# Performance work log

Hardware: AMD Instinct MI355X
Metric: run time of the kernel (lower is better)

## Reference

```python
import jax, jax.numpy as jnp
import numpy as np

N_NODES = 100000
N_EDGES = 3200000
F_IN = 256
H1 = 128   # growth_rate * bn_size
H2 = 32    # growth_rate
BN_EPS = 1e-5


def _gin_bn_relu(x, edge_index, Wa, ba, Wb, bb, gamma, beta):
    # GINConv (eps=0): h_i = MLP(x_i + sum_{j in N(i)} x_j)
    src, dst = edge_index[0], edge_index[1]
    agg = jax.ops.segment_sum(x[src], dst, num_segments=x.shape[0])  # [N, F]
    h = x + agg
    # nn1: Linear -> ReLU -> Linear
    h = jnp.maximum(h @ Wa + ba, 0.0)
    h = h @ Wb + bb
    # BatchNorm1d (training-mode batch stats over nodes)
    mean = h.mean(axis=0)
    var = h.var(axis=0)  # biased, matches torch BN normalization
    h = (h - mean) * jax.lax.rsqrt(var + BN_EPS) * gamma + beta
    return jnp.maximum(h, 0.0)


def setup_inputs() -> dict:
    key = jax.random.key(0)
    ks = jax.random.split(key, 12)
    x = jax.random.normal(ks[0], (N_NODES, F_IN), dtype=jnp.float32)
    edge_index = jax.random.randint(ks[1], (2, N_EDGES), 0, N_NODES, dtype=jnp.int64)

    def lin(k, fin, fout):
        s = 1.0 / np.sqrt(fin)
        return jax.random.uniform(k, (fin, fout), jnp.float32, -s, s)

    return {
        "x": x,
        "edge_index": edge_index,
        "W1a": lin(ks[2], F_IN, H1), "b1a": jnp.zeros((H1,), jnp.float32),
        "W1b": lin(ks[3], H1, H1),   "b1b": jnp.zeros((H1,), jnp.float32),
        "g1": jnp.ones((H1,), jnp.float32), "be1": jnp.zeros((H1,), jnp.float32),
        "W2a": lin(ks[4], H1, H2),   "b2a": jnp.zeros((H2,), jnp.float32),
        "W2b": lin(ks[5], H2, H2),   "b2b": jnp.zeros((H2,), jnp.float32),
        "g2": jnp.ones((H2,), jnp.float32), "be2": jnp.zeros((H2,), jnp.float32),
    }


def reference(x, edge_index, W1a, b1a, W1b, b1b, g1, be1,
              W2a, b2a, W2b, b2b, g2, be2):
    # data.x is a single tensor -> [x]; torch.cat([x], 1) == x (concat is a no-op)
    h = _gin_bn_relu(x, edge_index, W1a, b1a, W1b, b1b, g1, be1)   # [N, 128]
    h = _gin_bn_relu(h, edge_index, W2a, b2a, W2b, b2b, g2, be2)   # [N, 32]
    return h
```

## Files before the change

kernel.cpp:

```cpp
#include <hip/hip_runtime.h>

#define F_IN 256
#define H1 128
#define H2 32
#define BN_EPS 1e-5f
#define BSHIFT 8
#define BCAP 16384
#define CHUNK 4096
#define NSHARD 8

typedef short bf16x8 __attribute__((ext_vector_type(8)));
typedef float f32x4 __attribute__((ext_vector_type(4)));

__device__ __forceinline__ ushort f2bf(float f) {
    uint u = __float_as_uint(f);
    return (ushort)((u + 0x7FFFu + ((u >> 16) & 1u)) >> 16);
}
__device__ __forceinline__ float bf2f(ushort h) {
    return __uint_as_float((uint)h << 16);
}
__device__ __forceinline__ uint pack2(float a, float b) {
    return (uint)f2bf(a) | ((uint)f2bf(b) << 16);
}
__device__ __forceinline__ void unpack2(uint u, float& a, float& b) {
    a = __uint_as_float(u << 16);
    b = __uint_as_float(u & 0xFFFF0000u);
}
__device__ __forceinline__ int clampN(int v, int N) {
    return v < 0 ? 0 : (v >= N ? N - 1 : v);
}

__global__ __launch_bounds__(256) void super0_k(
    const float* __restrict__ W1a, const float* __restrict__ W1b,
    const float* __restrict__ W2a, const float* __restrict__ W2b,
    ushort* __restrict__ w1aT, ushort* __restrict__ w1bT,
    ushort* __restrict__ w2aT, ushort* __restrict__ w2bT,
    int* __restrict__ bucket_cursor, float* __restrict__ sums1,
    float* __restrict__ sums2) {
    const int tid = threadIdx.x;
    if (blockIdx.x == 212) {
        for (int i = tid; i < 512; i += 256) bucket_cursor[i] = 0;
        for (int i = tid; i < NSHARD * 2 * H1; i += 256) sums1[i] = 0.f;
        for (int i = tid; i < NSHARD * 2 * H2; i += 256) sums2[i] = 0.f;
        return;
    }
    int idx = blockIdx.x * 256 + tid;
    if (idx < 32768) {
        int k = idx >> 7, c = idx & 127;
        w1aT[c * 256 + k] = f2bf(W1a[idx]);
    } else if (idx < 49152) {
        int t = idx - 32768;
        int k = t >> 7, c = t & 127;
        w1bT[c * 128 + k] = f2bf(W1b[t]);
    } else if (idx < 53248) {
        int t = idx - 49152;
        int k = t >> 5, c = t & 31;
        w2aT[c * 128 + k] = f2bf(W2a[t]);
    } else if (idx < 54272) {
        int t = idx - 53248;
        int k = t >> 5, c = t & 31;
        w2bT[c * 32 + k] = f2bf(W2b[t]);
    }
}

__global__ __launch_bounds__(256) void binA_k(const int* __restrict__ eb,
                                              int E, int N, int NBUCK,
                                              int* __restrict__ bucket_cursor,
                                              uint* __restrict__ rec) {
    __shared__ int lcnt[512];
    __shared__ int lbase[512];
    __shared__ uint lrec[CHUNK];
    __shared__ ushort lbk[CHUNK];
    __shared__ ushort lrk[CHUNK];
    __shared__ int nzf;
    const int tid = threadIdx.x;
    const int cbase = blockIdx.x * CHUNK;
    const int cnum = min(CHUNK, E - cbase);
    if (cnum <= 0) return;
    if (tid == 0) nzf = 0;
    __syncthreads();
    {
        int i = tid * (CHUNK / 256);
        if (i < cnum && eb[2 * (cbase + i) + 1] != 0) atomicAdd(&nzf, 1);
    }
    for (int i = tid; i < NBUCK; i += 256) lcnt[i] = 0;
    __syncthreads();
    const int is64 = (nzf == 0);
    for (int i = tid; i < cnum; i += 256) {
        int e = cbase + i;
        int s = is64 ? eb[2 * e] : eb[e];
        int d = is64 ? eb[2 * (E + e)] : eb[E + e];
        s = clampN(s, N);
        d = clampN(d, N);
        int bk = d >> BSHIFT;
        int rk = atomicAdd(&lcnt[bk], 1);
        lrec[i] = (uint)s | ((uint)(d & 255) << 17);
        lbk[i] = (ushort)bk;
        lrk[i] = (ushort)rk;
    }
    __syncthreads();
    for (int i = tid; i < NBUCK; i += 256)
        if (lcnt[i]) lbase[i] = atomicAdd(&bucket_cursor[i], lcnt[i]);
    __syncthreads();
    for (int i = tid; i < cnum; i += 256) {
        int bk = lbk[i];
        int pos = lbase[bk] + lrk[i];
        if (pos < BCAP) rec[(size_t)bk * BCAP + pos] = lrec[i];
    }
}

__device__ __forceinline__ void binB_body(int bk, const uint* __restrict__ rec,
                                          const int* __restrict__ bucket_cursor,
                                          int N, int NBUCK,
                                          int* __restrict__ rs2,
                                          int* __restrict__ esrc) {
    __shared__ int cnt[2048];
    __shared__ int rnk[2048];
    __shared__ int red[256];
    const int tid = threadIdx.x;
    int part = 0;
    for (int i = tid; i < bk; i += 256) {
        int c = bucket_cursor[i];
        part += (c < BCAP) ? c : BCAP;
    }
    red[tid] = part;
    __syncthreads();
    for (int s = 128; s > 0; s >>= 1) {
        if (tid < s) red[tid] += red[tid + s];
        __syncthreads();
    }
    const int base = red[0];
    __syncthreads();
    int cntb = bucket_cursor[bk];
    if (cntb > BCAP) cntb = BCAP;
    if (bk == NBUCK - 1 && tid == 0) rs2[(size_t)N * 8] = base + cntb;

    const uint* r = rec + (size_t)bk * BCAP;
    for (int i = tid; i < 2048; i += 256) { cnt[i] = 0; rnk[i] = 0; }
    __syncthreads();
    for (int i = tid; i < cntb; i += 256) {
        uint rv = r[i];
        atomicAdd(&cnt[((rv >> 17) << 3) | ((rv >> 14) & 7u)], 1);
    }
    __syncthreads();
    int loc[8];
    int s = 0;
#pragma unroll
    for (int j = 0; j < 8; ++j) { loc[j] = s; s += cnt[tid * 8 + j]; }
    const int tot = s;
    red[tid] = tot;
    __syncthreads();
    for (int off = 1; off < 256; off <<= 1) {
        int t = (tid >= off) ? red[tid - off] : 0;
        __syncthreads();
        red[tid] += t;
        __syncthreads();
    }
    const int excl_t = red[tid] - tot;
    __syncthreads();
    const int n0 = bk << BSHIFT;
#pragma unroll
    for (int j = 0; j < 8; ++j) {
        int b = tid * 8 + j;
        int ex = excl_t + loc[j];
        cnt[b] = ex;
        int node = n0 + (b >> 3);
        if (node < N) rs2[(size_t)node * 8 + (b & 7)] = base + ex;
    }
    __syncthreads();
    for (int i = tid; i < cntb; i += 256) {
        uint rv = r[i];
        int b = ((rv >> 17) << 3) | ((rv >> 14) & 7u);
        int pos = cnt[b] + atomicAdd(&rnk[b], 1);
        esrc[base + pos] = (int)(rv & 0x1FFFFu);
    }
}

__device__ __forceinline__ void gemm1_body(int bid, const float* __restrict__ Af,
                                           const ushort* __restrict__ WT,
                                           ushort* __restrict__ outb, int N) {
    constexpr int K = F_IN, NC = H1, NF = NC / 16;
    const int lane = threadIdx.x & 63;
    const int wave = threadIdx.x >> 6;
    const int row0 = bid * 64 + wave * 16;
    const int col = lane & 15;
    const int k0 = (lane >> 4) * 8;
    int arow = row0 + col;
    if (arow >= N) arow = N - 1;

    f32x4 acc[NF];
#pragma unroll
    for (int f = 0; f < NF; ++f) acc[f] = (f32x4){0.f, 0.f, 0.f, 0.f};
#pragma unroll
    for (int kc = 0; kc < K; kc += 32) {
        const float* ap = &Af[(size_t)arow * K + kc + k0];
        float4 p = *(const float4*)ap;
        float4 q = *(const float4*)(ap + 4);
        bf16x8 af;
        af[0] = (short)f2bf(p.x); af[1] = (short)f2bf(p.y);
        af[2] = (short)f2bf(p.z); af[3] = (short)f2bf(p.w);
        af[4] = (short)f2bf(q.x); af[5] = (short)f2bf(q.y);
        af[6] = (short)f2bf(q.z); af[7] = (short)f2bf(q.w);
#pragma unroll
        for (int f = 0; f < NF; ++f) {
            bf16x8 bf = *(const bf16x8*)&WT[(size_t)(f * 16 + col) * K + kc + k0];
            acc[f] = __builtin_amdgcn_mfma_f32_16x16x32_bf16(af, bf, acc[f], 0, 0, 0);
        }
    }
    const int crow = row0 + (lane >> 4) * 4;
#pragma unroll
    for (int f = 0; f < NF; ++f) {
        const int c = f * 16 + col;
#pragma unroll
        for (int j = 0; j < 4; ++j) {
            int rr = crow + j;
            if (rr < N) outb[(size_t)rr * NC + c] = f2bf(acc[f][j]);
        }
    }
}

__global__ __launch_bounds__(256) void super2_k(
    const uint* __restrict__ rec, const int* __restrict__ bucket_cursor,
    int N, int NBUCK, int* __restrict__ rs2, int* __restrict__ esrc,
    const float* __restrict__ x, const ushort* __restrict__ w1aT,
    ushort* __restrict__ t1b) {
    if ((int)blockIdx.x < NBUCK)
        binB_body(blockIdx.x, rec, bucket_cursor, N, NBUCK, rs2, esrc);
    else
        gemm1_body(blockIdx.x - NBUCK, x, w1aT, t1b, N);
}

template <int NC, bool BIAS, bool OUT_BF16, bool STATS, int NF>
__device__ __forceinline__ void gemm_epilogue(f32x4* acc, const float* bias,
                                              void* outv, int N, int row0,
                                              int lane, float* sums) {
    __shared__ float ssum[NC];
    __shared__ float ssq[NC];
    if (STATS) {
        if (threadIdx.x < NC) { ssum[threadIdx.x] = 0.f; ssq[threadIdx.x] = 0.f; }
        __syncthreads();
    }
    const int col0 = lane & 15;
    const int crow = row0 + (lane >> 4) * 4;
#pragma unroll
    for (int f = 0; f < NF; ++f) {
        const int c = f * 16 + col0;
        float bv = BIAS ? bias[c] : 0.f;
        float sv = 0.f, qv = 0.f;
#pragma unroll
        for (int j = 0; j < 4; ++j) {
            int rr = crow + j;
            if (rr < N) {
                float v = acc[f][j] + bv;
                if (OUT_BF16) ((ushort*)outv)[(size_t)rr * NC + c] = f2bf(v);
                else          ((float*)outv)[(size_t)rr * NC + c] = v;
                if (STATS) { sv += v; qv += v * v; }
            }
        }
        if (STATS) {
            sv += __shfl_xor(sv, 16); sv += __shfl_xor(sv, 32);
            qv += __shfl_xor(qv, 16); qv += __shfl_xor(qv, 32);
            if ((lane >> 4) == 0) {
                atomicAdd(&ssum[c], sv);
                atomicAdd(&ssq[c], qv);
            }
        }
    }
    if (STATS) {
        __syncthreads();
        if (threadIdx.x < NC) {
            float* sh = sums + (blockIdx.x & (NSHARD - 1)) * 2 * NC;
            atomicAdd(&sh[threadIdx.x], ssum[threadIdx.x]);
            atomicAdd(&sh[NC + threadIdx.x], ssq[threadIdx.x]);
        }
    }
}

template <int K, int NC, bool BIAS, bool OUT_BF16, bool STATS>
__global__ __launch_bounds__(256) void gemm_mfma_k(const ushort* __restrict__ A,
                                                   const ushort* __restrict__ WT,
                                                   const float* __restrict__ bias,
                                                   void* __restrict__ outv, int N,
                                                   float* __restrict__ sums) {
    constexpr int NF = NC / 16;
    const int lane = threadIdx.x & 63;
    const int wave = threadIdx.x >> 6;
    const int row0 = blockIdx.x * 64 + wave * 16;
    const int col = lane & 15;
    const int k0 = (lane >> 4) * 8;
    int arow = row0 + col;
    if (arow >= N) arow = N - 1;

    f32x4 acc[NF];
#pragma unroll
    for (int f = 0; f < NF; ++f) acc[f] = (f32x4){0.f, 0.f, 0.f, 0.f};
#pragma unroll
    for (int kc = 0; kc < K; kc += 32) {
        bf16x8 af = *(const bf16x8*)&A[(size_t)arow * K + kc + k0];
#pragma unroll
        for (int f = 0; f < NF; ++f) {
            bf16x8 bf = *(const bf16x8*)&WT[(size_t)(f * 16 + col) * K + kc + k0];
            acc[f] = __builtin_amdgcn_mfma_f32_16x16x32_bf16(af, bf, acc[f], 0, 0, 0);
        }
    }
    gemm_epilogue<NC, BIAS, OUT_BF16, STATS, NF>(acc, bias, outv, N, row0, lane, sums);
}

template <int K, int NC, bool OUT_BF16>
__global__ __launch_bounds__(256) void gemm_mfma_bnA_k(const ushort* __restrict__ U,
                                                       const ushort* __restrict__ WT,
                                                       const float* __restrict__ sums,
                                                       const float* __restrict__ g,
                                                       const float* __restrict__ be,
                                                       int Nbn,
                                                       void* __restrict__ outv, int N) {
    constexpr int NF = NC / 16;
    __shared__ __align__(16) float lsc[K];
    __shared__ __align__(16) float lsh[K];
    const int tid = threadIdx.x;
    if (tid < K) {
        float s = 0.f, q = 0.f;
#pragma unroll
        for (int sh = 0; sh < NSHARD; ++sh) {
            s += sums[sh * 2 * K + tid];
            q += sums[sh * 2 * K + K + tid];
        }
        float inv_n = 1.f / (float)Nbn;
        float mean = s * inv_n;
        float var = q * inv_n - mean * mean;
        float sc = g[tid] * rsqrtf(var + BN_EPS);
        lsc[tid] = sc;
        lsh[tid] = be[tid] - mean * sc;
    }
    __syncthreads();

    const int lane = tid & 63;
    const int wave = tid >> 6;
    const int row0 = blockIdx.x * 64 + wave * 16;
    const int col = lane & 15;
    const int k0 = (lane >> 4) * 8;
    int arow = row0 + col;
    if (arow >= N) arow = N - 1;

    f32x4 acc[NF];
#pragma unroll
    for (int f = 0; f < NF; ++f) acc[f] = (f32x4){0.f, 0.f, 0.f, 0.f};
#pragma unroll
    for (int kc = 0; kc < K; kc += 32) {
        bf16x8 raw = *(const bf16x8*)&U[(size_t)arow * K + kc + k0];
        float4 c0 = *(const float4*)&lsc[kc + k0];
        float4 c1 = *(const float4*)&lsc[kc + k0 + 4];
        float4 h0 = *(const float4*)&lsh[kc + k0];
        float4 h1 = *(const float4*)&lsh[kc + k0 + 4];
        bf16x8 af;
        af[0] = (short)f2bf(fmaxf(bf2f((ushort)raw[0]) * c0.x + h0.x, 0.f));
        af[1] = (short)f2bf(fmaxf(bf2f((ushort)raw[1]) * c0.y + h0.y, 0.f));
        af[2] = (short)f2bf(fmaxf(bf2f((ushort)raw[2]) * c0.z + h0.z, 0.f));
        af[3] = (short)f2bf(fmaxf(bf2f((ushort)raw[3]) * c0.w + h0.w, 0.f));
        af[4] = (short)f2bf(fmaxf(bf2f((ushort)raw[4]) * c1.x + h1.x, 0.f));
        af[5] = (short)f2bf(fmaxf(bf2f((ushort)raw[5]) * c1.y + h1.y, 0.f));
        af[6] = (short)f2bf(fmaxf(bf2f((ushort)raw[6]) * c1.z + h1.z, 0.f));
        af[7] = (short)f2bf(fmaxf(bf2f((ushort)raw[7]) * c1.w + h1.w, 0.f));
#pragma unroll
        for (int f = 0; f < NF; ++f) {
            bf16x8 bf = *(const bf16x8*)&WT[(size_t)(f * 16 + col) * K + kc + k0];
            acc[f] = __builtin_amdgcn_mfma_f32_16x16x32_bf16(af, bf, acc[f], 0, 0, 0);
        }
    }
    gemm_epilogue<NC, false, OUT_BF16, false, NF>(acc, nullptr, outv, N, row0, lane, nullptr);
}

__global__ void agg_f128b_k(const ushort* __restrict__ T, const int* __restrict__ rs2,
                            const int* __restrict__ esrc, const float* __restrict__ bias,
                            ushort* __restrict__ out, int N) {
    const int hw = (blockIdx.x << 3) | (threadIdx.x >> 5);
    const int lane = threadIdx.x & 31;
    if (hw >= N) return;
    const uint2* T2 = (const uint2*)T;
    uint2 sv = T2[(size_t)hw * 32 + lane];
    float a0, a1, a2, a3;
    unpack2(sv.x, a0, a1);
    unpack2(sv.y, a2, a3);
    int p = rs2[(size_t)hw * 8];
    const int pe = rs2[(size_t)hw * 8 + 8];
    for (; p + 7 < pe; p += 8) {
        int s0 = esrc[p],     s1 = esrc[p + 1], s2 = esrc[p + 2], s3 = esrc[p + 3];
        int s4 = esrc[p + 4], s5 = esrc[p + 5], s6 = esrc[p + 6], s7 = esrc[p + 7];
        uint2 v0 = T2[(size_t)s0 * 32 + lane];
        uint2 v1 = T2[(size_t)s1 * 32 + lane];
        uint2 v2 = T2[(size_t)s2 * 32 + lane];
        uint2 v3 = T2[(size_t)s3 * 32 + lane];
        uint2 v4 = T2[(size_t)s4 * 32 + lane];
        uint2 v5 = T2[(size_t)s5 * 32 + lane];
        uint2 v6 = T2[(size_t)s6 * 32 + lane];
        uint2 v7 = T2[(size_t)s7 * 32 + lane];
        float x0, x1, x2, x3;
        unpack2(v0.x, x0, x1); unpack2(v0.y, x2, x3);
        a0 += x0; a1 += x1; a2 += x2; a3 += x3;
        unpack2(v1.x, x0, x1); unpack2(v1.y, x2, x3);
        a0 += x0; a1 += x1; a2 += x2; a3 += x3;
        unpack2(v2.x, x0, x1); unpack2(v2.y, x2, x3);
        a0 += x0; a1 += x1; a2 += x2; a3 += x3;
        unpack2(v3.x, x0, x1); unpack2(v3.y, x2, x3);
        a0 += x0; a1 += x1; a2 += x2; a3 += x3;
        unpack2(v4.x, x0, x1); unpack2(v4.y, x2, x3);
        a0 += x0; a1 += x1; a2 += x2; a3 += x3;
        unpack2(v5.x, x0, x1); unpack2(v5.y, x2, x3);
        a0 += x0; a1 += x1; a2 += x2; a3 += x3;
        unpack2(v6.x, x0, x1); unpack2(v6.y, x2, x3);
        a0 += x0; a1 += x1; a2 += x2; a3 += x3;
        unpack2(v7.x, x0, x1); unpack2(v7.y, x2, x3);
        a0 += x0; a1 += x1; a2 += x2; a3 += x3;
    }
    for (; p < pe; ++p) {
        uint2 v = T2[(size_t)esrc[p] * 32 + lane];
        float x0, x1, x2, x3;
        unpack2(v.x, x0, x1); unpack2(v.y, x2, x3);
        a0 += x0; a1 += x1; a2 += x2; a3 += x3;
    }
    const float4 b = ((const float4*)bias)[lane];
    a0 = fmaxf(a0 + b.x, 0.f);
    a1 = fmaxf(a1 + b.y, 0.f);
    a2 = fmaxf(a2 + b.z, 0.f);
    a3 = fmaxf(a3 + b.w, 0.f);
    ((uint2*)out)[(size_t)hw * 32 + lane] = make_uint2(pack2(a0, a1), pack2(a2, a3));
}

__global__ void agg_f32b_k(const ushort* __restrict__ T, const int* __restrict__ rs2,
                           const int* __restrict__ esrc, const float* __restrict__ bias,
                           ushort* __restrict__ out, int N) {
    const int wid = (blockIdx.x << 2) | (threadIdx.x >> 6);
    const int lane = threadIdx.x & 63;
    const int g = lane >> 3, l8 = lane & 7;
    if (wid >= N) return;
    const uint2* T2 = (const uint2*)T;
    float a0 = 0.f, a1 = 0.f, a2 = 0.f, a3 = 0.f;
    const int p0 = rs2[(size_t)wid * 8];
    const int pe = rs2[(size_t)wid * 8 + 8];
    for (int p = p0 + g; p < pe; p += 8) {
        uint2 v = T2[(size_t)esrc[p] * 8 + l8];
        float x0, x1, x2, x3;
        unpack2(v.x, x0, x1); unpack2(v.y, x2, x3);
        a0 += x0; a1 += x1; a2 += x2; a3 += x3;
    }
#pragma unroll
    for (int off = 8; off < 64; off <<= 1) {
        a0 += __shfl_xor(a0, off);
        a1 += __shfl_xor(a1, off);
        a2 += __shfl_xor(a2, off);
        a3 += __shfl_xor(a3, off);
    }
    if (g == 0) {
        uint2 sv = T2[(size_t)wid * 8 + l8];
        float s0, s1, s2, s3;
        unpack2(sv.x, s0, s1); unpack2(sv.y, s2, s3);
        const float4 b = ((const float4*)bias)[l8];
        a0 = fmaxf(a0 + s0 + b.x, 0.f);
        a1 = fmaxf(a1 + s1 + b.y, 0.f);
        a2 = fmaxf(a2 + s2 + b.z, 0.f);
        a3 = fmaxf(a3 + s3 + b.w, 0.f);
        ((uint2*)out)[(size_t)wid * 8 + l8] = make_uint2(pack2(a0, a1), pack2(a2, a3));
    }
}

template <int F>
__global__ void bnapply_fin_k(const float* __restrict__ U, const float* __restrict__ sums,
                              const float* __restrict__ g, const float* __restrict__ be,
                              int Nbn, float* __restrict__ out, int total4) {
    __shared__ __align__(16) float lsc[F];
    __shared__ __align__(16) float lsh[F];
    const int tid = threadIdx.x;
    if (tid < F) {
        float s = 0.f, q = 0.f;
#pragma unroll
        for (int sh = 0; sh < NSHARD; ++sh) {
            s += sums[sh * 2 * F + tid];
            q += sums[sh * 2 * F + F + tid];
        }
        float inv_n = 1.f / (float)Nbn;
        float mean = s * inv_n;
        float var = q * inv_n - mean * mean;
        float sc = g[tid] * rsqrtf(var + BN_EPS);
        lsc[tid] = sc;
        lsh[tid] = be[tid] - mean * sc;
    }
    __syncthreads();
    const float4* U4 = (const float4*)U;
    float4* O4 = (float4*)out;
    const int stride = gridDim.x * blockDim.x;
    for (int i = blockIdx.x * blockDim.x + tid; i < total4; i += stride) {
        int c4 = (i % (F / 4)) * 4;
        float4 u = U4[i];
        float4 sc = *(const float4*)&lsc[c4];
        float4 sh = *(const float4*)&lsh[c4];
        float4 o;
        o.x = fmaxf(u.x * sc.x + sh.x, 0.f);
        o.y = fmaxf(u.y * sc.y + sh.y, 0.f);
        o.z = fmaxf(u.z * sc.z + sh.z, 0.f);
        o.w = fmaxf(u.w * sc.w + sh.w, 0.f);
        O4[i] = o;
    }
}

extern "C" void kernel_launch(void* const* d_in, const int* in_sizes, int n_in,
                              void* d_out, int out_size, void* d_ws, size_t ws_size,
                              hipStream_t stream) {
    const float* x   = (const float*)d_in[0];
    const int*   eb  = (const int*)d_in[1];
    const float* W1a = (const float*)d_in[2];
    const float* b1a = (const float*)d_in[3];
    const float* W1b = (const float*)d_in[4];
    const float* b1b = (const float*)d_in[5];
    const float* g1  = (const float*)d_in[6];
    const float* be1 = (const float*)d_in[7];
    const float* W2a = (const float*)d_in[8];
    const float* b2a = (const float*)d_in[9];
    const float* W2b = (const float*)d_in[10];
    const float* b2b = (const float*)d_in[11];
    const float* g2  = (const float*)d_in[12];
    const float* be2 = (const float*)d_in[13];
    float* out = (float*)d_out;

    const int N = in_sizes[0] / F_IN;
    const int E = in_sizes[1] / 2;
    const int NBUCK = (N + 255) >> BSHIFT;

    char* w = (char*)d_ws;
    size_t off = 0;
    auto alloc = [&](size_t bytes) -> void* {
        void* p = w + off;
        off = (off + bytes + 255) & ~(size_t)255;
        return p;
    };
    ushort* B0 = (ushort*)alloc((size_t)N * H1 * 2);
    ushort* B1 = (ushort*)alloc((size_t)N * H1 * 2);
    char*   B2 = (char*)alloc((size_t)N * H1 * 4);
    ushort* u1b = (ushort*)B2;
    float*  u2  = (float*)B2;

    int* rs2       = (int*)alloc(((size_t)N * 8 + 1) * 4);
    int* esrc      = (int*)alloc((size_t)E * 4);
    uint* rec      = (uint*)alloc((size_t)NBUCK * BCAP * 4);
    int* bucket_cursor = (int*)alloc(512 * 4);
    ushort* w1aT = (ushort*)alloc(F_IN * H1 * 2);
    ushort* w1bT = (ushort*)alloc(H1 * H1 * 2);
    ushort* w2aT = (ushort*)alloc(H1 * H2 * 2);
    ushort* w2bT = (ushort*)alloc(H2 * H2 * 2);
    float* sums1 = (float*)alloc(NSHARD * 2 * H1 * 4);
    float* sums2 = (float*)alloc(NSHARD * 2 * H2 * 4);

    const int GB = (E + CHUNK - 1) / CHUNK;
    const int G1 = (N + 63) / 64;

    super0_k<<<213, 256, 0, stream>>>(W1a, W1b, W2a, W2b, w1aT, w1bT, w2aT, w2bT,
                                      bucket_cursor, sums1, sums2);
    binA_k<<<GB, 256, 0, stream>>>(eb, E, N, NBUCK, bucket_cursor, rec);
    super2_k<<<NBUCK + G1, 256, 0, stream>>>(rec, bucket_cursor, N, NBUCK,
                                             rs2, esrc, x, w1aT, B1);
    agg_f128b_k<<<(N + 7) / 8, 256, 0, stream>>>(B1, rs2, esrc, b1a, B0, N);
    gemm_mfma_k<H1, H1, true, true, true><<<G1, 256, 0, stream>>>(B0, w1bT, b1b, u1b, N, sums1);
    gemm_mfma_bnA_k<H1, H2, true><<<G1, 256, 0, stream>>>(u1b, w2aT, sums1, g1, be1, N, B1, N);
    agg_f32b_k<<<(N + 3) / 4, 256, 0, stream>>>(B1, rs2, esrc, b2a, B0, N);
    gemm_mfma_k<H2, H2, true, false, true><<<G1, 256, 0, stream>>>(B0, w2bT, b2b, u2, N, sums2);
    bnapply_fin_k<H2><<<3125, 256, 0, stream>>>(u2, sums2, g2, be2, N, out, N * H2 / 4);
}
```

Baseline: 370.2 us.

## Make layer-1 aggregation persistent, processing node groups in source-range phases

The first-layer gather kernel now runs on a fixed grid of 1792 blocks. Each half-wave handles up to 7 consecutive nodes and walks their edges in four phases, using the per-node sub-range offsets in rs2 (which appear to split edges by source range). The idea is to make concurrent waves touch the same slice of the feature table together, improving L2/MALL hit rates for the random gathers. The self term is added in the epilogue, and a 4-edge unrolled tail is added. The risks are more registers for seven accumulators, reduced memory-level parallelism per wave, and load imbalance from the fixed grid.

```diff
diff --git a/kernel.cpp b/kernel.cpp
--- a/kernel.cpp
+++ b/kernel.cpp
@@ -8,6 +8,7 @@
 #define BCAP 16384
 #define CHUNK 4096
 #define NSHARD 8
+#define AGG1_GRID 1792
 
 typedef short bf16x8 __attribute__((ext_vector_type(8)));
 typedef float f32x4 __attribute__((ext_vector_type(4)));
@@ -370,60 +371,98 @@
     gemm_epilogue<NC, false, OUT_BF16, false, NF>(acc, nullptr, outv, N, row0, lane, nullptr);
 }
 
-__global__ void agg_f128b_k(const ushort* __restrict__ T, const int* __restrict__ rs2,
-                            const int* __restrict__ esrc, const float* __restrict__ bias,
-                            ushort* __restrict__ out, int N) {
-    const int hw = (blockIdx.x << 3) | (threadIdx.x >> 5);
+__global__ __launch_bounds__(256, 7) void agg_f128b_k(
+    const ushort* __restrict__ T, const int* __restrict__ rs2,
+    const int* __restrict__ esrc, const float* __restrict__ bias,
+    ushort* __restrict__ out, int N, int NPH) {
+    const int hw = blockIdx.x * 8 + (threadIdx.x >> 5);
     const int lane = threadIdx.x & 31;
-    if (hw >= N) return;
+    const int nbase = hw * NPH;
+    if (nbase >= N) return;
     const uint2* T2 = (const uint2*)T;
-    uint2 sv = T2[(size_t)hw * 32 + lane];
-    float a0, a1, a2, a3;
-    unpack2(sv.x, a0, a1);
-    unpack2(sv.y, a2, a3);
-    int p = rs2[(size_t)hw * 8];
-    const int pe = rs2[(size_t)hw * 8 + 8];
-    for (; p + 7 < pe; p += 8) {
-        int s0 = esrc[p],     s1 = esrc[p + 1], s2 = esrc[p + 2], s3 = esrc[p + 3];
-        int s4 = esrc[p + 4], s5 = esrc[p + 5], s6 = esrc[p + 6], s7 = esrc[p + 7];
-        uint2 v0 = T2[(size_t)s0 * 32 + lane];
-        uint2 v1 = T2[(size_t)s1 * 32 + lane];
-        uint2 v2 = T2[(size_t)s2 * 32 + lane];
-        uint2 v3 = T2[(size_t)s3 * 32 + lane];
-        uint2 v4 = T2[(size_t)s4 * 32 + lane];
-        uint2 v5 = T2[(size_t)s5 * 32 + lane];
-        uint2 v6 = T2[(size_t)s6 * 32 + lane];
-        uint2 v7 = T2[(size_t)s7 * 32 + lane];
-        float x0, x1, x2, x3;
-        unpack2(v0.x, x0, x1); unpack2(v0.y, x2, x3);
-        a0 += x0; a1 += x1; a2 += x2; a3 += x3;
-        unpack2(v1.x, x0, x1); unpack2(v1.y, x2, x3);
-        a0 += x0; a1 += x1; a2 += x2; a3 += x3;
-        unpack2(v2.x, x0, x1); unpack2(v2.y, x2, x3);
-        a0 += x0; a1 += x1; a2 += x2; a3 += x3;
-        unpack2(v3.x, x0, x1); unpack2(v3.y, x2, x3);
-        a0 += x0; a1 += x1; a2 += x2; a3 += x3;
-        unpack2(v4.x, x0, x1); unpack2(v4.y, x2, x3);
-        a0 += x0; a1 += x1; a2 += x2; a3 += x3;
-        unpack2(v5.x, x0, x1); unpack2(v5.y, x2, x3);
-        a0 += x0; a1 += x1; a2 += x2; a3 += x3;
-        unpack2(v6.x, x0, x1); unpack2(v6.y, x2, x3);
-        a0 += x0; a1 += x1; a2 += x2; a3 += x3;
-        unpack2(v7.x, x0, x1); unpack2(v7.y, x2, x3);
-        a0 += x0; a1 += x1; a2 += x2; a3 += x3;
-    }
-    for (; p < pe; ++p) {
-        uint2 v = T2[(size_t)esrc[p] * 32 + lane];
-        float x0, x1, x2, x3;
-        unpack2(v.x, x0, x1); unpack2(v.y, x2, x3);
-        a0 += x0; a1 += x1; a2 += x2; a3 += x3;
+    f32x4 acc[7];
+#pragma unroll
+    for (int j = 0; j < 7; ++j) acc[j] = (f32x4){0.f, 0.f, 0.f, 0.f};
+
+    for (int ph = 0; ph < 4; ++ph) {
+#pragma unroll
+        for (int j = 0; j < 7; ++j) {
+            int node = nbase + j;
+            if (j < NPH && node < N) {
+                int p = rs2[(size_t)node * 8 + ph * 2];
+                const int pe = rs2[(size_t)node * 8 + ph * 2 + 2];
+                float a0 = acc[j][0], a1 = acc[j][1], a2 = acc[j][2], a3 = acc[j][3];
+                for (; p + 7 < pe; p += 8) {
+                    int s0 = esrc[p],     s1 = esrc[p + 1], s2 = esrc[p + 2], s3 = esrc[p + 3];
+                    int s4 = esrc[p + 4], s5 = esrc[p + 5], s6 = esrc[p + 6], s7 = esrc[p + 7];
+                    uint2 v0 = T2[(size_t)s0 * 32 + lane];
+                    uint2 v1 = T2[(size_t)s1 * 32 + lane];
+                    uint2 v2 = T2[(size_t)s2 * 32 + lane];
+                    uint2 v3 = T2[(size_t)s3 * 32 + lane];
+                    uint2 v4 = T2[(size_t)s4 * 32 + lane];
+                    uint2 v5 = T2[(size_t)s5 * 32 + lane];
+                    uint2 v6 = T2[(size_t)s6 * 32 + lane];
+                    uint2 v7 = T2[(size_t)s7 * 32 + lane];
+                    float x0, x1, x2, x3;
+                    unpack2(v0.x, x0, x1); unpack2(v0.y, x2, x3);
+                    a0 += x0; a1 += x1; a2 += x2; a3 += x3;
+                    unpack2(v1.x, x0, x1); unpack2(v1.y, x2, x3);
+                    a0 += x0; a1 += x1; a2 += x2; a3 += x3;
+                    unpack2(v2.x, x0, x1); unpack2(v2.y, x2, x3);
+                    a0 += x0; a1 += x1; a2 += x2; a3 += x3;
+                    unpack2(v3.x, x0, x1); unpack2(v3.y, x2, x3);
+                    a0 += x0; a1 += x1; a2 += x2; a3 += x3;
+                    unpack2(v4.x, x0, x1); unpack2(v4.y, x2, x3);
+                    a0 += x0; a1 += x1; a2 += x2; a3 += x3;
+                    unpack2(v5.x, x0, x1); unpack2(v5.y, x2, x3);
+                    a0 += x0; a1 += x1; a2 += x2; a3 += x3;
+                    unpack2(v6.x, x0, x1); unpack2(v6.y, x2, x3);
+                    a0 += x0; a1 += x1; a2 += x2; a3 += x3;
+                    unpack2(v7.x, x0, x1); unpack2(v7.y, x2, x3);
+                    a0 += x0; a1 += x1; a2 += x2; a3 += x3;
+                }
+                if (p + 3 < pe) {
+                    int s0 = esrc[p], s1 = esrc[p + 1], s2 = esrc[p + 2], s3 = esrc[p + 3];
+                    uint2 v0 = T2[(size_t)s0 * 32 + lane];
+                    uint2 v1 = T2[(size_t)s1 * 32 + lane];
+                    uint2 v2 = T2[(size_t)s2 * 32 + lane];
+                    uint2 v3 = T2[(size_t)s3 * 32 + lane];
+                    float x0, x1, x2, x3;
+                    unpack2(v0.x, x0, x1); unpack2(v0.y, x2, x3);
+                    a0 += x0; a1 += x1; a2 += x2; a3 += x3;
+                    unpack2(v1.x, x0, x1); unpack2(v1.y, x2, x3);
+                    a0 += x0; a1 += x1; a2 += x2; a3 += x3;
+                    unpack2(v2.x, x0, x1); unpack2(v2.y, x2, x3);
+                    a0 += x0; a1 += x1; a2 += x2; a3 += x3;
+                    unpack2(v3.x, x0, x1); unpack2(v3.y, x2, x3);
+                    a0 += x0; a1 += x1; a2 += x2; a3 += x3;
+                    p += 4;
+                }
+                for (; p < pe; ++p) {
+                    uint2 v = T2[(size_t)esrc[p] * 32 + lane];
+                    float x0, x1, x2, x3;
+                    unpack2(v.x, x0, x1); unpack2(v.y, x2, x3);
+                    a0 += x0; a1 += x1; a2 += x2; a3 += x3;
+                }
+                acc[j][0] = a0; acc[j][1] = a1; acc[j][2] = a2; acc[j][3] = a3;
+            }
+        }
     }
     const float4 b = ((const float4*)bias)[lane];
-    a0 = fmaxf(a0 + b.x, 0.f);
-    a1 = fmaxf(a1 + b.y, 0.f);
-    a2 = fmaxf(a2 + b.z, 0.f);
-    a3 = fmaxf(a3 + b.w, 0.f);
-    ((uint2*)out)[(size_t)hw * 32 + lane] = make_uint2(pack2(a0, a1), pack2(a2, a3));
+#pragma unroll
+    for (int j = 0; j < 7; ++j) {
+        int node = nbase + j;
+        if (j < NPH && node < N) {
+            uint2 sv = T2[(size_t)node * 32 + lane];
+            float s0, s1, s2, s3;
+            unpack2(sv.x, s0, s1); unpack2(sv.y, s2, s3);
+            float o0 = fmaxf(acc[j][0] + s0 + b.x, 0.f);
+            float o1 = fmaxf(acc[j][1] + s1 + b.y, 0.f);
+            float o2 = fmaxf(acc[j][2] + s2 + b.z, 0.f);
+            float o3 = fmaxf(acc[j][3] + s3 + b.w, 0.f);
+            ((uint2*)out)[(size_t)node * 32 + lane] = make_uint2(pack2(o0, o1), pack2(o2, o3));
+        }
+    }
 }
 
 __global__ void agg_f32b_k(const ushort* __restrict__ T, const int* __restrict__ rs2,
@@ -551,13 +590,15 @@
 
     const int GB = (E + CHUNK - 1) / CHUNK;
     const int G1 = (N + 63) / 64;
+    const int HWT = AGG1_GRID * 8;
+    const int NPH = (N + HWT - 1) / HWT;
 
     super0_k<<<213, 256, 0, stream>>>(W1a, W1b, W2a, W2b, w1aT, w1bT, w2aT, w2bT,
                                       bucket_cursor, sums1, sums2);
     binA_k<<<GB, 256, 0, stream>>>(eb, E, N, NBUCK, bucket_cursor, rec);
     super2_k<<<NBUCK + G1, 256, 0, stream>>>(rec, bucket_cursor, N, NBUCK,
                                              rs2, esrc, x, w1aT, B1);
-    agg_f128b_k<<<(N + 7) / 8, 256, 0, stream>>>(B1, rs2, esrc, b1a, B0, N);
+    agg_f128b_k<<<AGG1_GRID, 256, 0, stream>>>(B1, rs2, esrc, b1a, B0, N, NPH);
     gemm_mfma_k<H1, H1, true, true, true><<<G1, 256, 0, stream>>>(B0, w1bT, b1b, u1b, N, sums1);
     gemm_mfma_bnA_k<H1, H2, true><<<G1, 256, 0, stream>>>(u1b, w2aT, sums1, g1, be1, N, B1, N);
     agg_f32b_k<<<(N + 3) / 4, 256, 0, stream>>>(B1, rs2, esrc, b2a, B0, N);
```

Measured after the change: 382.6 us. +3.3%, slower.
